# Kernel optimization log

Hardware: AMD Instinct MI355X
Metric: run time of the kernel (lower is better)

Reference implementation:

```python
import jax, jax.numpy as jnp
import numpy as np

V, D, H, L, T_MAX = 95, 384, 6, 6, 256
HD = D // H  # 64
FF = 4 * D


def _layernorm(x, scale, bias, eps=1e-5):
    m = jnp.mean(x, axis=-1, keepdims=True)
    v = jnp.var(x, axis=-1, keepdims=True)
    return (x - m) * jax.lax.rsqrt(v + eps) * scale + bias


def setup_inputs() -> dict:
    key = jax.random.key(0)
    ks = iter(jax.random.split(key, 32))
    std = 0.02
    p = {
        "idx": jax.random.randint(next(ks), (128, 256), 0, V, dtype=jnp.int64)
               if jax.config.jax_enable_x64 else
               jax.random.randint(next(ks), (128, 256), 0, V, dtype=jnp.int32),
        "tok_emb": jax.random.normal(next(ks), (V, D), jnp.float32) * std,
        "pos_emb": jax.random.normal(next(ks), (T_MAX, D), jnp.float32) * std,
        # per-layer stacked params [L, ...]
        "ln1_s": jnp.ones((L, D), jnp.float32),
        "ln1_b": jnp.zeros((L, D), jnp.float32),
        "wq": jax.random.normal(next(ks), (L, D, D), jnp.float32) * std,
        "wk": jax.random.normal(next(ks), (L, D, D), jnp.float32) * std,
        "wv": jax.random.normal(next(ks), (L, D, D), jnp.float32) * std,
        "wo": jax.random.normal(next(ks), (L, D, D), jnp.float32) * std,
        "bo": jnp.zeros((L, D), jnp.float32),
        "ln2_s": jnp.ones((L, D), jnp.float32),
        "ln2_b": jnp.zeros((L, D), jnp.float32),
        "w1": jax.random.normal(next(ks), (L, D, FF), jnp.float32) * std,
        "b1": jnp.zeros((L, FF), jnp.float32),
        "w2": jax.random.normal(next(ks), (L, FF, D), jnp.float32) * std,
        "b2": jnp.zeros((L, D), jnp.float32),
        "lnf_s": jnp.ones((D,), jnp.float32),
        "lnf_b": jnp.zeros((D,), jnp.float32),
        "head_w": jax.random.normal(next(ks), (D, V), jnp.float32) * std,
        "head_b": jnp.zeros((V,), jnp.float32),
    }
    return p


def reference(idx, tok_emb, pos_emb, ln1_s, ln1_b, wq, wk, wv, wo, bo,
              ln2_s, ln2_b, w1, b1, w2, b2, lnf_s, lnf_b, head_w, head_b):
    B, T = idx.shape
    x = tok_emb[idx] + pos_emb[:T]  # [B,T,D]
    mask = jnp.tril(jnp.ones((T, T), bool))  # causal
    scale = HD ** -0.5

    def block(x, p):
        s1, b1n, Wq, Wk, Wv, Wo, Bo, s2, b2n, W1, B1, W2, B2 = p
        h = _layernorm(x, s1, b1n)
        q = (h @ Wq).reshape(B, T, H, HD)
        k = (h @ Wk).reshape(B, T, H, HD)
        v = (h @ Wv).reshape(B, T, H, HD)
        scores = jnp.einsum('bqhd,bkhd->bhqk', q, k) * scale
        scores = jnp.where(mask, scores, -jnp.inf)
        wei = jax.nn.softmax(scores, axis=-1)
        attn = jnp.einsum('bhqk,bkhd->bqhd', wei, v).reshape(B, T, D)
        x = x + attn @ Wo + Bo
        h2 = _layernorm(x, s2, b2n)
        x = x + jax.nn.relu(h2 @ W1 + B1) @ W2 + B2
        return x, None

    x, _ = jax.lax.scan(block, x, (ln1_s, ln1_b, wq, wk, wv, wo, bo,
                                   ln2_s, ln2_b, w1, b1, w2, b2))
    logits = _layernorm(x, lnf_s, lnf_b) @ head_w + head_b  # [B,T,V]
    return logits
```

## Files before the change

### kernel.cpp

```cpp
#include <hip/hip_runtime.h>
#include <hip/hip_bf16.h>
#include <cstdint>

#define DEV __device__ __forceinline__

typedef __hip_bfloat16 bf16;
typedef unsigned short u16;
typedef unsigned int u32;
typedef __attribute__((ext_vector_type(8))) short s8v;
typedef __attribute__((ext_vector_type(4))) float f4;

static constexpr int Bn = 128;
static constexpr int Tn = 256;
static constexpr int Dn = 384;
static constexpr int Hn = 6;
static constexpr int HDn = 64;
static constexpr int FFn = 1536;
static constexpr int Vn = 95;
static constexpr int Mn = Bn * 256;

DEV u16 f2b(float f) {
  bf16 h = __float2bfloat16(f);
  return *reinterpret_cast<u16*>(&h);
}
DEV u32 pk2(float a, float b) { return (u32)f2b(a) | ((u32)f2b(b) << 16); }

DEV void gl_lds16(const void* g, void* l) {
  auto gp = (const __attribute__((address_space(1))) u32*)(uintptr_t)g;
  auto lp = (__attribute__((address_space(3))) u32*)(u32)(uintptr_t)l;
  __builtin_amdgcn_global_load_lds(gp, lp, 16, 0, 0);
}

template <int MODE, bool RELU, int NKT, int NT>
__global__ __launch_bounds__(256) void gemm_h(
    const u16* __restrict__ A, const u16* __restrict__ Bw,
    const float* __restrict__ bias, const float* __restrict__ resid,
    void* __restrict__ outp)
{
  constexpr int K = NKT * 64;
  constexpr int N = NT * 16;
  constexpr int nTiles = NT / 8;
  __shared__ __align__(16) u16 As[3][128 * 64];
  const int tid = threadIdx.x;
  const int lane = tid & 63, wave = tid >> 6;
  const int quad = lane >> 4, l16 = lane & 15;
  const int wy = wave >> 1, wx = wave & 1;
  const int blk = blockIdx.x;
  const int xcd = blk & 7, tt = blk >> 3;
  const int nT = tt % nTiles, mT = xcd + 8 * (tt / nTiles);
  const int mBase = mT * 128, nBase = nT * 128;

  f4 acc[4][4] = {};

  int rS[4], cS[4];
#pragma unroll
  for (int i = 0; i < 4; i++) {
    int s = i * 256 + tid;
    rS[i] = s >> 3;
    cS[i] = ((s & 7) ^ (rS[i] & 7)) * 8;
  }

  const u16* Ab = A + (size_t)mBase * K;
  const u16* Bp = Bw + (size_t)((nBase >> 4) + wx * 4) * 512 + lane * 8;

#define STAGEA(buf, kt)                                                       \
  do {                                                                        \
    _Pragma("unroll")                                                         \
    for (int i = 0; i < 4; i++)                                               \
      gl_lds16(Ab + (size_t)rS[i] * K + (kt) + cS[i],                         \
               &As[buf][(i * 256 + wave * 64) * 8]);                          \
  } while (0)

  STAGEA(0, 0);
  STAGEA(1, 64);
  const int nk = NKT;
#pragma unroll
  for (int ik = 0; ik < nk; ik++) {
    const int cur = ik % 3;
    asm volatile("s_barrier" ::: "memory");
    s8v bq[8];
#pragma unroll
    for (int ks = 0; ks < 2; ks++)
#pragma unroll
      for (int j = 0; j < 4; j++)
        bq[ks * 4 + j] = *(const s8v*)(Bp + (size_t)(ik * 2 + ks) * (NT * 512) + j * 512);
    __builtin_amdgcn_sched_barrier(0);
    if (ik + 2 < nk) {
      STAGEA((ik + 2) % 3, (ik + 2) * 64);
      asm volatile("s_waitcnt vmcnt(16)" ::: "memory");
    } else if (ik + 1 < nk) {
      asm volatile("s_waitcnt vmcnt(12)" ::: "memory");
    } else {
      asm volatile("s_waitcnt vmcnt(8)" ::: "memory");
    }
    asm volatile("s_barrier" ::: "memory");
#pragma unroll
    for (int ks = 0; ks < 2; ks++) {
      s8v af[4];
#pragma unroll
      for (int i = 0; i < 4; i++) {
        int row = wy * 64 + i * 16 + l16;
        int ch = (ks * 4 + quad) ^ (row & 7);
        af[i] = *(const s8v*)&As[cur][row * 64 + ch * 8];
      }
#pragma unroll
      for (int i = 0; i < 4; i++)
#pragma unroll
        for (int j = 0; j < 4; j++)
          acc[i][j] = __builtin_amdgcn_mfma_f32_16x16x32_bf16(af[i], bq[ks * 4 + j], acc[i][j], 0, 0, 0);
    }
  }
#undef STAGEA

  if (MODE == 0) {
    u16* out = (u16*)outp;
#pragma unroll
    for (int j = 0; j < 4; j++) {
      int n = nBase + wx * 64 + j * 16 + l16;
      float bv = bias ? bias[n] : 0.f;
#pragma unroll
      for (int i = 0; i < 4; i++) {
        int m0 = mBase + wy * 64 + i * 16 + quad * 4;
#pragma unroll
        for (int r = 0; r < 4; r++) {
          float v = acc[i][j][r] + bv;
          if (RELU) v = fmaxf(v, 0.f);
          out[(size_t)(m0 + r) * N + n] = f2b(v);
        }
      }
    }
  } else if (MODE == 1) {
    float* out = (float*)outp;
#pragma unroll
    for (int j = 0; j < 4; j++) {
      int n = nBase + wx * 64 + j * 16 + l16;
      float bv = bias[n];
#pragma unroll
      for (int i = 0; i < 4; i++) {
        int m0 = mBase + wy * 64 + i * 16 + quad * 4;
#pragma unroll
        for (int r = 0; r < 4; r++) {
          int m = m0 + r;
          out[(size_t)m * N + n] = resid[(size_t)m * N + n] + acc[i][j][r] + bv;
        }
      }
    }
  } else if (MODE == 3) {
    float* out = (float*)outp;
#pragma unroll
    for (int j = 0; j < 4; j++) {
      int n = nBase + wx * 64 + j * 16 + l16;
      if (n < Vn) {
        float bv = bias[n];
#pragma unroll
        for (int i = 0; i < 4; i++) {
          int m0 = mBase + wy * 64 + i * 16 + quad * 4;
#pragma unroll
          for (int r = 0; r < 4; r++)
            out[(size_t)(m0 + r) * Vn + n] = acc[i][j][r] + bv;
        }
      }
    }
  } else if (MODE == 4) {
    u16* qb = (u16*)outp;
    u16* kb = qb + (size_t)Mn * 384;
    u16* vb = kb + (size_t)Mn * 384;
#pragma unroll
    for (int j = 0; j < 4; j++) {
      int n = nBase + wx * 64 + j * 16 + l16;
      if (n < 768) {
        u16* dst = (n < 384) ? qb : kb;
        int col = (n < 384) ? n : (n - 384);
#pragma unroll
        for (int i = 0; i < 4; i++) {
          int m0 = mBase + wy * 64 + i * 16 + quad * 4;
#pragma unroll
          for (int r = 0; r < 4; r++)
            dst[(size_t)(m0 + r) * 384 + col] = f2b(acc[i][j][r]);
        }
      } else {
        int n7 = n - 768;
        int hh = n7 >> 6, d = n7 & 63;
#pragma unroll
        for (int i = 0; i < 4; i++) {
          int m0 = mBase + wy * 64 + i * 16 + quad * 4;
          int b = m0 >> 8, t0 = m0 & 255;
          uint2 w;
          w.x = pk2(acc[i][j][0], acc[i][j][1]);
          w.y = pk2(acc[i][j][2], acc[i][j][3]);
          *(uint2*)&vb[((b * Hn + hh) * HDn + d) * Tn + t0] = w;
        }
      }
    }
  }
}

__global__ __launch_bounds__(256) void attn_kernel(
    const u16* __restrict__ q, const u16* __restrict__ k,
    const u16* __restrict__ vT, u16* __restrict__ ao)
{
  __shared__ __align__(16) u16 Ps[4][2][16 * 40];
  const int tid = threadIdx.x, lane = tid & 63, wave = tid >> 6;
  const int quad = lane >> 4, l16 = lane & 15;
  const int c4 = blockIdx.x / 768;
  const int bh = blockIdx.x - c4 * 768;
  const int b = bh / Hn, h = bh % Hn;
  const u16* qg = q + (b * Tn) * Dn + h * HDn;
  const u16* kg = k + (b * Tn) * Dn + h * HDn;
  const u16* vg = vT + bh * (HDn * Tn);
  u16* aog = ao + (b * Tn) * Dn + h * HDn;
  const float c1 = 0.125f * 1.44269504f;

  const int qt = (wave & 2) ? ((wave & 1) ? 15 - c4 : 8 + c4)
                            : ((wave & 1) ? 7 - c4 : c4);
  const int qglob = qt * 16 + l16;

  const s8v qf0 = *(const s8v*)&qg[qglob * Dn + quad * 8];
  const s8v qf1 = *(const s8v*)&qg[qglob * Dn + 32 + quad * 8];

  float lsum = 0.f;
  f4 O[4] = {};

  const int nch = qt / 2 + 1;
  for (int c2 = 0; c2 < nch; c2++) {
    const int kk0 = c2 * 32;
    f4 S0 = {0.f, 0.f, 0.f, 0.f}, S1 = S0;
    {
      s8v kf = *(const s8v*)&kg[(kk0 + l16) * Dn + quad * 8];
      S0 = __builtin_amdgcn_mfma_f32_16x16x32_bf16(kf, qf0, S0, 0, 0, 0);
      kf = *(const s8v*)&kg[(kk0 + l16) * Dn + 32 + quad * 8];
      S0 = __builtin_amdgcn_mfma_f32_16x16x32_bf16(kf, qf1, S0, 0, 0, 0);
    }
    if (kk0 + 16 <= qt * 16) {
      s8v kf = *(const s8v*)&kg[(kk0 + 16 + l16) * Dn + quad * 8];
      S1 = __builtin_amdgcn_mfma_f32_16x16x32_bf16(kf, qf0, S1, 0, 0, 0);
      kf = *(const s8v*)&kg[(kk0 + 16 + l16) * Dn + 32 + quad * 8];
      S1 = __builtin_amdgcn_mfma_f32_16x16x32_bf16(kf, qf1, S1, 0, 0, 0);
    }
    const int kkq = kk0 + quad * 4;
    f4 E0, E1;
#pragma unroll
    for (int r = 0; r < 4; r++) {
      E0[r] = (kkq + r <= qglob) ? exp2f(S0[r] * c1) : 0.f;
      E1[r] = (kkq + 16 + r <= qglob) ? exp2f(S1[r] * c1) : 0.f;
      lsum += E0[r] + E1[r];
    }
    u16* prow = &Ps[wave][c2 & 1][l16 * 40];
    uint2 w0, w1;
    w0.x = pk2(E0[0], E0[1]); w0.y = pk2(E0[2], E0[3]);
    w1.x = pk2(E1[0], E1[1]); w1.y = pk2(E1[2], E1[3]);
    *(uint2*)&prow[quad * 4] = w0;
    *(uint2*)&prow[16 + quad * 4] = w1;
    const s8v pf = *(const s8v*)&prow[quad * 8];
#pragma unroll
    for (int dm = 0; dm < 4; dm++) {
      s8v vf = *(const s8v*)&vg[(dm * 16 + l16) * Tn + kk0 + quad * 8];
      O[dm] = __builtin_amdgcn_mfma_f32_16x16x32_bf16(vf, pf, O[dm], 0, 0, 0);
    }
  }

  lsum += __shfl_xor(lsum, 16);
  lsum += __shfl_xor(lsum, 32);
  const float inv = 1.0f / lsum;
#pragma unroll
  for (int dm = 0; dm < 4; dm++) {
    uint2 w;
    w.x = pk2(O[dm][0] * inv, O[dm][1] * inv);
    w.y = pk2(O[dm][2] * inv, O[dm][3] * inv);
    *(uint2*)&aog[qglob * Dn + dm * 16 + quad * 4] = w;
  }
}

__global__ __launch_bounds__(256) void ln_kernel(
    const float* __restrict__ x, const float* __restrict__ sc,
    const float* __restrict__ bi, u16* __restrict__ out)
{
  int tok = blockIdx.x * 4 + (threadIdx.x >> 6);
  int lane = threadIdx.x & 63;
  const float* xr = x + (size_t)tok * Dn;
  float v[6];
  float s = 0.f, sq = 0.f;
#pragma unroll
  for (int i = 0; i < 6; i++) {
    v[i] = xr[lane + 64 * i];
    s += v[i];
    sq += v[i] * v[i];
  }
#pragma unroll
  for (int o = 1; o < 64; o <<= 1) {
    s += __shfl_xor(s, o);
    sq += __shfl_xor(sq, o);
  }
  float mean = s * (1.f / 384.f);
  float var = sq * (1.f / 384.f) - mean * mean;
  float inv = rsqrtf(var + 1e-5f);
  u16* orow = out + (size_t)tok * Dn;
#pragma unroll
  for (int i = 0; i < 6; i++) {
    int c = lane + 64 * i;
    orow[c] = f2b((v[i] - mean) * inv * sc[c] + bi[c]);
  }
}

__global__ __launch_bounds__(256) void embed_kernel(
    const int* __restrict__ idx, const float* __restrict__ tok,
    const float* __restrict__ pos, float* __restrict__ x)
{
  int i = blockIdx.x * 256 + threadIdx.x;
  int m = i / 96, c = (i - m * 96) * 4;
  int t = m & (Tn - 1);
  const float4 tv = *(const float4*)&tok[idx[m] * Dn + c];
  const float4 pv = *(const float4*)&pos[t * Dn + c];
  float4 r;
  r.x = tv.x + pv.x; r.y = tv.y + pv.y; r.z = tv.z + pv.z; r.w = tv.w + pv.w;
  *(float4*)&x[m * Dn + c] = r;
}

__global__ __launch_bounds__(256) void tcvt_frag(
    const float* __restrict__ src, u16* __restrict__ dst,
    int K, int C, int NTsub, int NTtot, int ntoff, int total)
{
  int t = blockIdx.x * 256 + threadIdx.x;
  if (t >= total) return;
  int j8 = t & 7;
  int lane = (t >> 3) & 63;
  int rest = t >> 9;
  int nt = rest % NTsub;
  int lkc = rest / NTsub;
  int KC = K >> 5;
  int kc = lkc % KC;
  int l = lkc / KC;
  int quad = lane >> 4, l16 = lane & 15;
  int k = kc * 32 + quad * 8 + j8;
  int n = nt * 16 + l16;
  float v = (n < C) ? src[((size_t)l * K + k) * C + n] : 0.f;
  dst[((size_t)(l * KC + kc) * NTtot + ntoff + nt) * 512 + lane * 8 + j8] = f2b(v);
}

extern "C" void kernel_launch(void* const* d_in, const int* in_sizes, int n_in,
                              void* d_out, int out_size, void* d_ws, size_t ws_size,
                              hipStream_t stream)
{
  (void)in_sizes; (void)n_in; (void)out_size;
  const int*   idx     = (const int*)d_in[0];
  const float* tok_emb = (const float*)d_in[1];
  const float* pos_emb = (const float*)d_in[2];
  const float* ln1_s   = (const float*)d_in[3];
  const float* ln1_b   = (const float*)d_in[4];
  const float* wq      = (const float*)d_in[5];
  const float* wk      = (const float*)d_in[6];
  const float* wv      = (const float*)d_in[7];
  const float* wo      = (const float*)d_in[8];
  const float* bo      = (const float*)d_in[9];
  const float* ln2_s   = (const float*)d_in[10];
  const float* ln2_b   = (const float*)d_in[11];
  const float* w1      = (const float*)d_in[12];
  const float* b1      = (const float*)d_in[13];
  const float* w2      = (const float*)d_in[14];
  const float* b2      = (const float*)d_in[15];
  const float* lnf_s   = (const float*)d_in[16];
  const float* lnf_b   = (const float*)d_in[17];
  const float* head_w  = (const float*)d_in[18];
  const float* head_b  = (const float*)d_in[19];
  float* out = (float*)d_out;

  char* ws = (char*)d_ws;
  float* x  = (float*)(ws + 0);
  u16*   h  = (u16*)(ws + 50331648);
  u16*   qb = (u16*)(ws + 75497472);
  u16*   kb = (u16*)(ws + 100663296);
  u16*   vb = (u16*)(ws + 125829120);
  u16*   ab = (u16*)(ws + 150994944);
  u16*   f1 = qb;
  u16* qkvT = (u16*)(ws + 176160768);
  u16* woT  = qkvT + 6 * 442368;
  u16* w1T  = woT + 6 * 147456;
  u16* w2T  = w1T + 6 * 589824;
  u16* hdT  = w2T + 6 * 589824;
  if (ws_size < (size_t)197492736) return;

  int tot = 6 * 384 * 384;
  tcvt_frag<<<(tot + 255) / 256, 256, 0, stream>>>(wq, qkvT, 384, 384, 24, 72, 0, tot);
  tcvt_frag<<<(tot + 255) / 256, 256, 0, stream>>>(wk, qkvT, 384, 384, 24, 72, 24, tot);
  tcvt_frag<<<(tot + 255) / 256, 256, 0, stream>>>(wv, qkvT, 384, 384, 24, 72, 48, tot);
  tcvt_frag<<<(tot + 255) / 256, 256, 0, stream>>>(wo, woT, 384, 384, 24, 24, 0, tot);
  tot = 6 * 384 * 1536;
  tcvt_frag<<<(tot + 255) / 256, 256, 0, stream>>>(w1, w1T, 384, 1536, 96, 96, 0, tot);
  tcvt_frag<<<(tot + 255) / 256, 256, 0, stream>>>(w2, w2T, 1536, 384, 24, 24, 0, tot);
  tot = 384 * 128;
  tcvt_frag<<<(tot + 255) / 256, 256, 0, stream>>>(head_w, hdT, 384, 95, 8, 8, 0, tot);

  embed_kernel<<<(Mn * 96) / 256, 256, 0, stream>>>(idx, tok_emb, pos_emb, x);

  for (int l = 0; l < 6; l++) {
    ln_kernel<<<Mn / 4, 256, 0, stream>>>(x, ln1_s + l * Dn, ln1_b + l * Dn, h);
    gemm_h<4, false, 6, 72><<<2304, 256, 0, stream>>>(h, qkvT + l * 442368, nullptr, nullptr, qb);
    attn_kernel<<<Bn * Hn * 4, 256, 0, stream>>>(qb, kb, vb, ab);
    gemm_h<1, false, 6, 24><<<768, 256, 0, stream>>>(ab, woT + l * 147456, bo + l * Dn, x, x);
    ln_kernel<<<Mn / 4, 256, 0, stream>>>(x, ln2_s + l * Dn, ln2_b + l * Dn, h);
    gemm_h<0, true, 6, 96><<<3072, 256, 0, stream>>>(h, w1T + l * 589824, b1 + l * FFn, nullptr, f1);
    gemm_h<1, false, 24, 24><<<768, 256, 0, stream>>>(f1, w2T + l * 589824, b2 + l * Dn, x, x);
  }
  ln_kernel<<<Mn / 4, 256, 0, stream>>>(x, lnf_s, lnf_b, h);
  gemm_h<3, false, 6, 8><<<256, 256, 0, stream>>>(h, hdT, head_b, nullptr, out);
}
```

Baseline: 1.665 ms.

## Software-pipeline B-fragment loads across k-steps and drop a barrier per iteration

Restructures the GEMM main loop so the first half of each k-tile's B fragments is prefetched one iteration ahead into double-buffered registers. The second half is loaded just before use, with fine-grained vmcnt waits so MFMAs on the first half overlap the remaining loads. This removes one of the two s_barriers per k-iteration. It also adds a min-blocks hint of 2 to launch_bounds, which caps registers to raise occupancy but risks spills given the extra register buffers.

After: 1.602 ms. 3.8% less time.

```diff
diff --git a/kernel.cpp b/kernel.cpp
--- a/kernel.cpp
+++ b/kernel.cpp
@@ -31,8 +31,14 @@
   __builtin_amdgcn_global_load_lds(gp, lp, 16, 0, 0);
 }
 
+DEV void waitvm(int n) {
+  if (n == 0)      asm volatile("s_waitcnt vmcnt(0)" ::: "memory");
+  else if (n == 4) asm volatile("s_waitcnt vmcnt(4)" ::: "memory");
+  else if (n == 8) asm volatile("s_waitcnt vmcnt(8)" ::: "memory");
+}
+
 template <int MODE, bool RELU, int NKT, int NT>
-__global__ __launch_bounds__(256) void gemm_h(
+__global__ __launch_bounds__(256, 2) void gemm_h(
     const u16* __restrict__ A, const u16* __restrict__ Bw,
     const float* __restrict__ bias, const float* __restrict__ resid,
     void* __restrict__ outp)
@@ -71,43 +77,64 @@
                &As[buf][(i * 256 + wave * 64) * 8]);                          \
   } while (0)
 
+  s8v bqa[2][4];
   STAGEA(0, 0);
+  __builtin_amdgcn_sched_barrier(0);
+#pragma unroll
+  for (int j = 0; j < 4; j++)
+    bqa[0][j] = *(const s8v*)(Bp + (size_t)0 * (NT * 512) + j * 512);
+  __builtin_amdgcn_sched_barrier(0);
   STAGEA(1, 64);
+  __builtin_amdgcn_sched_barrier(0);
+
   const int nk = NKT;
 #pragma unroll
   for (int ik = 0; ik < nk; ik++) {
     const int cur = ik % 3;
+    const int par = ik & 1;
+    waitvm((ik + 1 < nk) ? 4 : 0);
     asm volatile("s_barrier" ::: "memory");
-    s8v bq[8];
-#pragma unroll
-    for (int ks = 0; ks < 2; ks++)
+    s8v bqb[4];
+#pragma unroll
+    for (int j = 0; j < 4; j++)
+      bqb[j] = *(const s8v*)(Bp + (size_t)(ik * 2 + 1) * (NT * 512) + j * 512);
+    __builtin_amdgcn_sched_barrier(0);
+    if (ik + 1 < nk) {
 #pragma unroll
       for (int j = 0; j < 4; j++)
-        bq[ks * 4 + j] = *(const s8v*)(Bp + (size_t)(ik * 2 + ks) * (NT * 512) + j * 512);
+        bqa[par ^ 1][j] = *(const s8v*)(Bp + (size_t)(ik * 2 + 2) * (NT * 512) + j * 512);
+    }
     __builtin_amdgcn_sched_barrier(0);
-    if (ik + 2 < nk) {
-      STAGEA((ik + 2) % 3, (ik + 2) * 64);
-      asm volatile("s_waitcnt vmcnt(16)" ::: "memory");
-    } else if (ik + 1 < nk) {
-      asm volatile("s_waitcnt vmcnt(12)" ::: "memory");
-    } else {
-      asm volatile("s_waitcnt vmcnt(8)" ::: "memory");
-    }
-    asm volatile("s_barrier" ::: "memory");
-#pragma unroll
-    for (int ks = 0; ks < 2; ks++) {
+    if (ik + 2 < nk) STAGEA((ik + 2) % 3, (ik + 2) * 64);
+    __builtin_amdgcn_sched_barrier(0);
+    {
       s8v af[4];
 #pragma unroll
       for (int i = 0; i < 4; i++) {
         int row = wy * 64 + i * 16 + l16;
-        int ch = (ks * 4 + quad) ^ (row & 7);
+        int ch = quad ^ (row & 7);
         af[i] = *(const s8v*)&As[cur][row * 64 + ch * 8];
       }
 #pragma unroll
       for (int i = 0; i < 4; i++)
 #pragma unroll
         for (int j = 0; j < 4; j++)
-          acc[i][j] = __builtin_amdgcn_mfma_f32_16x16x32_bf16(af[i], bq[ks * 4 + j], acc[i][j], 0, 0, 0);
+          acc[i][j] = __builtin_amdgcn_mfma_f32_16x16x32_bf16(af[i], bqa[par][j], acc[i][j], 0, 0, 0);
+    }
+    waitvm(4 * ((ik + 1 < nk) + (ik + 2 < nk)));
+    {
+      s8v af[4];
+#pragma unroll
+      for (int i = 0; i < 4; i++) {
+        int row = wy * 64 + i * 16 + l16;
+        int ch = (4 + quad) ^ (row & 7);
+        af[i] = *(const s8v*)&As[cur][row * 64 + ch * 8];
+      }
+#pragma unroll
+      for (int i = 0; i < 4; i++)
+#pragma unroll
+        for (int j = 0; j < 4; j++)
+          acc[i][j] = __builtin_amdgcn_mfma_f32_16x16x32_bf16(af[i], bqb[j], acc[i][j], 0, 0, 0);
     }
   }
 #undef STAGEA
```
